# Optimization experiments

Hardware: AMD Instinct MI355X
Metric: run time of the kernel (lower is better)

Reference implementation:

```python
import jax, jax.numpy as jnp
import numpy as np

EMBED_DIM = 1024
NUM_HEADS = 16
HEAD_DIM = EMBED_DIM // NUM_HEADS  # 64
B, H_P, W_P = 4, 48, 48
N = H_P * W_P  # 2304


def setup_inputs() -> dict:
    key = jax.random.key(0)
    ks = jax.random.split(key, 12)
    s = 1.0 / np.sqrt(EMBED_DIM)
    inp = {
        "query": jax.random.normal(ks[0], (B, N, EMBED_DIM), jnp.float32),
        "key": jax.random.normal(ks[1], (B, N, EMBED_DIM), jnp.float32),
        "value": jax.random.normal(ks[2], (B, N, EMBED_DIM), jnp.float32),
        "Wq": jax.random.normal(ks[3], (EMBED_DIM, EMBED_DIM), jnp.float32) * s,
        "bq": jnp.zeros((EMBED_DIM,), jnp.float32),
        "Wk": jax.random.normal(ks[4], (EMBED_DIM, EMBED_DIM), jnp.float32) * s,
        "bk": jnp.zeros((EMBED_DIM,), jnp.float32),
        "Wv": jax.random.normal(ks[5], (EMBED_DIM, EMBED_DIM), jnp.float32) * s,
        "bv": jnp.zeros((EMBED_DIM,), jnp.float32),
        "Wo": jax.random.normal(ks[6], (EMBED_DIM, EMBED_DIM), jnp.float32) * s,
        "bo": jnp.zeros((EMBED_DIM,), jnp.float32),
        "H_patch": H_P,
        "W_patch": W_P,
    }
    return inp


def _rope_2d_cos_sin(h_idx, w_idx, head_dim):
    # 2D RoPE: first half of head_dim encodes the y axis, second half the x axis.
    half = head_dim // 2          # dims per spatial axis (32)
    inv_freq = 1.0 / (10000.0 ** (jnp.arange(0, half, 2, dtype=jnp.float32) / half))  # [half//2]
    fh = h_idx.astype(jnp.float32)[:, None] * inv_freq[None, :]  # [N, half//2]
    fw = w_idx.astype(jnp.float32)[:, None] * inv_freq[None, :]
    emb_h = jnp.concatenate([fh, fh], axis=-1)  # [N, half]
    emb_w = jnp.concatenate([fw, fw], axis=-1)
    emb = jnp.concatenate([emb_h, emb_w], axis=-1)  # [N, head_dim]
    return jnp.cos(emb), jnp.sin(emb)


def _rotate_half_seg(x):
    # rotate_half within a per-axis segment
    h = x.shape[-1] // 2
    return jnp.concatenate([-x[..., h:], x[..., :h]], axis=-1)


def _apply_rotary_2d(x, cos, sin):
    # x: [B, H, N, head_dim]; cos/sin: [N, head_dim]
    half = x.shape[-1] // 2
    c = cos[None, None]
    s = sin[None, None]
    xh, xw = x[..., :half], x[..., half:]
    ch, cw = c[..., :half], c[..., half:]
    sh, sw = s[..., :half], s[..., half:]
    yh = xh * ch + _rotate_half_seg(xh) * sh
    yw = xw * cw + _rotate_half_seg(xw) * sw
    return jnp.concatenate([yh, yw], axis=-1)


def reference(query, key, value, Wq, bq, Wk, bk, Wv, bv, Wo, bo, H_patch, W_patch):
    Bsz, Nn, D = query.shape
    hd = D // NUM_HEADS

    def split_heads(x):
        return x.reshape(Bsz, Nn, NUM_HEADS, hd).transpose(0, 2, 1, 3)  # [B,H,N,hd]

    q = split_heads(query @ Wq.T + bq)
    k = split_heads(key @ Wk.T + bk)
    v = split_heads(value @ Wv.T + bv)

    ys = jnp.arange(H_patch)
    xs = jnp.arange(W_patch)
    yy, xx = jnp.meshgrid(ys, xs, indexing="ij")
    cos, sin = _rope_2d_cos_sin(yy.reshape(-1), xx.reshape(-1), hd)

    q = _apply_rotary_2d(q, cos, sin)
    k = _apply_rotary_2d(k, cos, sin)

    scale = hd ** (-0.5)
    attn = jnp.einsum("bhnd,bhmd->bhnm", q, k) * scale
    attn = jax.nn.softmax(attn, axis=-1)
    out = jnp.einsum("bhnm,bhmd->bhnd", attn, v)
    out = out.transpose(0, 2, 1, 3).reshape(Bsz, Nn, D)
    return out @ Wo.T + bo
```

## Files before the change

### kernel.cpp

```cpp
#include <hip/hip_runtime.h>
#include <cstdint>
#include <cstddef>


typedef __bf16 bf16x8 __attribute__((ext_vector_type(8)));
typedef __bf16 bf16x4 __attribute__((ext_vector_type(4)));
typedef _Float16 f16x4 __attribute__((ext_vector_type(4)));
typedef float f32x4 __attribute__((ext_vector_type(4)));

constexpr int Bc = 4, Hc = 16, Nc = 2304, Ec = 1024, WPc = 48;
constexpr int BNc = Bc * Nc;

__device__ __forceinline__ f32x4 mfma16(bf16x8 a, bf16x8 b, f32x4 c) {
  return __builtin_amdgcn_mfma_f32_16x16x32_bf16(a, b, c, 0, 0, 0);
}
__device__ __forceinline__ f32x4 mfmah(f16x4 a, f16x4 b, f32x4 c) {
  return __builtin_amdgcn_mfma_f32_16x16x16f16(a, b, c, 0, 0, 0);
}

#define GPTR(p) ((const __attribute__((address_space(1))) void*)(p))
#define LPTR(p) ((__attribute__((address_space(3))) void*)(p))

__global__ __launch_bounds__(256) void cvt_bf16(const float* __restrict__ s,
                                                __bf16* __restrict__ d, int n) {
  int i = (blockIdx.x * 256 + threadIdx.x) * 8;
  if (i >= n) return;
  float4 f0 = *(const float4*)(s + i);
  float4 f1 = *(const float4*)(s + i + 4);
  bf16x8 v;
  v[0] = (__bf16)f0.x; v[1] = (__bf16)f0.y; v[2] = (__bf16)f0.z; v[3] = (__bf16)f0.w;
  v[4] = (__bf16)f1.x; v[5] = (__bf16)f1.y; v[6] = (__bf16)f1.z; v[7] = (__bf16)f1.w;
  *(bf16x8*)(d + i) = v;
}

#define GEMM_CORE(APTR, WPTR, KDIM)                                             \
  __shared__ __align__(16) __bf16 As[128 * 32];                                 \
  __shared__ __align__(16) __bf16 Bs[128 * 32];                                 \
  const int t = threadIdx.x;                                                    \
  const int lane = t & 63, wave = t >> 6;                                       \
  const int wm = wave & 1, wn = wave >> 1;                                      \
  const int quad = lane >> 4, l15 = lane & 15;                                  \
  const int rowInC = lane >> 2, colC = (lane & 3) * 8;                          \
  const __bf16* Ab = (APTR) + (size_t)(tm * 128) * (KDIM);                      \
  const __bf16* Wb = (WPTR) + (size_t)(tn * 128) * (KDIM);                      \
  f32x4 zero = {0.f, 0.f, 0.f, 0.f};                                            \
  f32x4 acc[4][4];                                                              \
  for (int i = 0; i < 4; ++i)                                                   \
    for (int j = 0; j < 4; ++j) acc[i][j] = zero;                               \
  for (int kk = 0; kk < (KDIM); kk += 32) {                                     \
    _Pragma("unroll") for (int tch = 0; tch < 2; ++tch) {                       \
      const int ch = wave * 2 + tch;                                            \
      const int row = ch * 16 + rowInC;                                         \
      __builtin_amdgcn_global_load_lds(GPTR(Ab + (size_t)row * (KDIM) + kk + colC), \
                                       LPTR(As + ch * 512), 16, 0, 0);          \
      __builtin_amdgcn_global_load_lds(GPTR(Wb + (size_t)row * (KDIM) + kk + colC), \
                                       LPTR(Bs + ch * 512), 16, 0, 0);          \
    }                                                                           \
    __syncthreads();                                                            \
    bf16x8 af[4], bfg[4];                                                       \
    _Pragma("unroll") for (int i = 0; i < 4; ++i)                               \
        af[i] = *(const bf16x8*)(As + (wm * 64 + i * 16 + l15) * 32 + quad * 8);\
    _Pragma("unroll") for (int j = 0; j < 4; ++j)                               \
        bfg[j] = *(const bf16x8*)(Bs + (wn * 64 + j * 16 + l15) * 32 + quad * 8);\
    _Pragma("unroll") for (int i = 0; i < 4; ++i)                               \
      _Pragma("unroll") for (int j = 0; j < 4; ++j)                             \
        acc[i][j] = mfma16(af[i], bfg[j], acc[i][j]);                           \
    __syncthreads();                                                            \
  }                                                                             \
  const int m0 = tm * 128 + wm * 64;                                            \
  const int nb0 = tn * 128 + wn * 64;

__global__ __launch_bounds__(256) void gemm_qk(const __bf16* __restrict__ qkb,
                                               const __bf16* __restrict__ Wqk,
                                               const float* __restrict__ bq,
                                               const float* __restrict__ bk,
                                               __bf16* __restrict__ Qhp,
                                               __bf16* __restrict__ Khp,
                                               float qscale) {
  const int tn = blockIdx.x & 15;
  const int tm = blockIdx.x >> 4;
  const int proj = tn >> 3;
  const __bf16* Asel = qkb + (size_t)proj * BNc * Ec;
  GEMM_CORE(Asel, Wqk, Ec)

  const int h = (nb0 >> 6) & 15;
  const float scale = proj ? 1.0f : qscale;
  __bf16* O = proj ? Khp : Qhp;
  const float* bb = proj ? bk : bq;
  float bj[4];
#pragma unroll
  for (int j = 0; j < 4; ++j) bj[j] = bb[(nb0 + j * 16 + l15) & 1023];
  const float f = exp2f(-(float)l15 * 0.8304820237218406f);
  const int lo3 = l15 & 7, hi8 = l15 >> 3;
#pragma unroll
  for (int i = 0; i < 4; ++i) {
#pragma unroll
    for (int r = 0; r < 4; ++r) {
      const int m = m0 + i * 16 + quad * 4 + r;
      const int b = m / Nc;
      const int ntok = m - b * Nc;
      const int ph = ntok / WPc, pw = ntok - (ntok / WPc) * WPc;
      float sh, ch, sw, cw;
      __sincosf((float)ph * f, &sh, &ch);
      __sincosf((float)pw * f, &sw, &cw);
      const float x0 = acc[i][0][r] + bj[0];
      const float x1 = acc[i][1][r] + bj[1];
      const float x2 = acc[i][2][r] + bj[2];
      const float x3 = acc[i][3][r] + bj[3];
      __bf16* Op = O + ((size_t)(b * Hc + h) * Nc + ntok) * 64;
      const int n7 = proj ? (ntok & 7) : 0;
      Op[(((0 + hi8) ^ n7) << 3) | lo3] = (__bf16)((x0 * ch - x1 * sh) * scale);
      Op[(((2 + hi8) ^ n7) << 3) | lo3] = (__bf16)((x1 * ch + x0 * sh) * scale);
      Op[(((4 + hi8) ^ n7) << 3) | lo3] = (__bf16)((x2 * cw - x3 * sw) * scale);
      Op[(((6 + hi8) ^ n7) << 3) | lo3] = (__bf16)((x3 * cw + x2 * sw) * scale);
    }
  }
}

__global__ __launch_bounds__(256) void gemm_v(const __bf16* __restrict__ A,
                                              const __bf16* __restrict__ Wv,
                                              const float* __restrict__ bv,
                                              _Float16* __restrict__ Vt) {
  const int tn = blockIdx.x & 7;
  const int tm = blockIdx.x >> 3;
  GEMM_CORE(A, Wv, Ec)

  const int h = nb0 >> 6;
#pragma unroll
  for (int i = 0; i < 4; ++i) {
    const int m = m0 + i * 16 + quad * 4;
    const int b = m / Nc;
    const int ntok = m - b * Nc;
    const int seg = ntok >> 6;
    const int cw = (ntok >> 2) & 15;
#pragma unroll
    for (int j = 0; j < 4; ++j) {
      const int d = j * 16 + l15;
      const float bi = bv[nb0 + j * 16 + l15];
      f16x4 v;
#pragma unroll
      for (int r = 0; r < 4; ++r) v[r] = (_Float16)(acc[i][j][r] + bi);
      const int off = seg * 64 + (((cw ^ l15) & 15) << 2);
      *(f16x4*)(Vt + ((size_t)(b * Hc + h) * 64 + d) * Nc + off) = v;
    }
  }
}

__global__ __launch_bounds__(256) void gemm_out(const __bf16* __restrict__ A,
                                                const __bf16* __restrict__ Wo,
                                                const float* __restrict__ bo,
                                                float* __restrict__ C) {
  const int tn = blockIdx.x & 7;
  const int tm = blockIdx.x >> 3;
  GEMM_CORE(A, Wo, Ec)

#pragma unroll
  for (int j = 0; j < 4; ++j) {
    const int n = nb0 + j * 16 + l15;
    const float bi = bo[n];
#pragma unroll
    for (int i = 0; i < 4; ++i) {
      const int m = m0 + i * 16 + quad * 4;
#pragma unroll
      for (int r = 0; r < 4; ++r) C[(size_t)(m + r) * Ec + n] = acc[i][j][r] + bi;
    }
  }
}

constexpr int TQ = 128, TK = 64, NT = Nc / TK;

__global__ __launch_bounds__(256) void attn(const __bf16* __restrict__ Qh,
                                            const __bf16* __restrict__ Kg,
                                            const _Float16* __restrict__ Vg,
                                            __bf16* __restrict__ Om) {
  const int bh = blockIdx.x;
  const int t = threadIdx.x, wave = t >> 6, lane = t & 63;
  const int quad = lane >> 4, l15 = lane & 15;

  __shared__ __align__(16) __bf16 Kls[2][TK * 64];
  __shared__ __align__(16) _Float16 Vls[2][TK * 64];

  const int qbase = blockIdx.y * TQ + wave * 32;
  bf16x8 bq[2][2];
#pragma unroll
  for (int s = 0; s < 2; ++s)
#pragma unroll
    for (int ks = 0; ks < 2; ++ks)
      bq[s][ks] = *(const bf16x8*)(Qh + ((size_t)bh * Nc + qbase + s * 16 + l15) * 64 +
                                   ks * 32 + quad * 8);

  const __bf16* Kbh = Kg + (size_t)bh * Nc * 64;
  const _Float16* Vbh = Vg + (size_t)bh * 64 * Nc;

  const f32x4 zero = {0.f, 0.f, 0.f, 0.f};
  f32x4 oacc[2][4] = {{zero, zero, zero, zero}, {zero, zero, zero, zero}};
  f32x4 osum[2] = {zero, zero};
  const f16x4 fones = {(_Float16)1.f, (_Float16)1.f, (_Float16)1.f, (_Float16)1.f};

  const int vrow = lane >> 3, vcol = (lane & 7) * 8;

#define STAGE(kt, buf)                                                          \
  {                                                                             \
    _Pragma("unroll") for (int i = 0; i < 2; ++i) {                             \
      const int ch = wave * 2 + i;                                              \
      __builtin_amdgcn_global_load_lds(                                         \
          GPTR(Kbh + (size_t)(kt) * TK * 64 + ch * 512 + lane * 8),             \
          LPTR(&Kls[buf][ch * 512]), 16, 0, 0);                                 \
    }                                                                           \
    _Pragma("unroll") for (int i = 0; i < 2; ++i) {                             \
      const int ch = wave * 2 + i;                                              \
      const int d = ch * 8 + vrow;                                              \
      __builtin_amdgcn_global_load_lds(                                         \
          GPTR(Vbh + (size_t)d * Nc + (kt) * 64 + vcol),                        \
          LPTR(&Vls[buf][ch * 512]), 16, 0, 0);                                 \
    }                                                                           \
  }

#define COMPUTE(BUF)                                                            \
  {                                                                             \
    f32x4 sacc[2][4] = {{zero, zero, zero, zero}, {zero, zero, zero, zero}};    \
    _Pragma("unroll") for (int ks = 0; ks < 2; ++ks) {                          \
      _Pragma("unroll") for (int ct = 0; ct < 4; ++ct) {                        \
        const bf16x8 ak = *(const bf16x8*)(&Kls[BUF][(ct * 16 + l15) * 64 +     \
            (((ks * 4 + quad) ^ (l15 & 7)) << 3)]);                             \
        sacc[0][ct] = mfma16(ak, bq[0][ks], sacc[0][ct]);                       \
        sacc[1][ct] = mfma16(ak, bq[1][ks], sacc[1][ct]);                       \
      }                                                                         \
    }                                                                           \
    f16x4 pf[2][4];                                                             \
    _Pragma("unroll") for (int s = 0; s < 2; ++s)                               \
      _Pragma("unroll") for (int ct = 0; ct < 4; ++ct)                          \
        _Pragma("unroll") for (int r = 0; r < 4; ++r)                           \
          pf[s][ct][r] = (_Float16)exp2f(sacc[s][ct][r]);                       \
    _Pragma("unroll") for (int ct = 0; ct < 4; ++ct) {                          \
      _Pragma("unroll") for (int dt = 0; dt < 4; ++dt) {                        \
        const f16x4 av = *(const f16x4*)(&Vls[BUF][(dt * 16 + l15) * 64 +       \
            (((ct * 4 + quad) ^ l15) << 2)]);                                   \
        oacc[0][dt] = mfmah(av, pf[0][ct], oacc[0][dt]);                        \
        oacc[1][dt] = mfmah(av, pf[1][ct], oacc[1][dt]);                        \
      }                                                                         \
      osum[0] = mfmah(fones, pf[0][ct], osum[0]);                               \
      osum[1] = mfmah(fones, pf[1][ct], osum[1]);                               \
    }                                                                           \
  }

  STAGE(0, 0);
  __syncthreads();

  for (int kt = 0; kt < NT; kt += 2) {
    STAGE(kt + 1, 1);
    COMPUTE(0)
    __syncthreads();
    if (kt + 2 < NT) STAGE(kt + 2, 0);
    COMPUTE(1)
    __syncthreads();
  }

  const int b = bh >> 4, h = bh & 15;
#pragma unroll
  for (int s = 0; s < 2; ++s) {
    const float rinv = 1.0f / osum[s][0];
    __bf16* Op = Om + ((size_t)b * Nc + qbase + s * 16 + l15) * Ec + h * 64 + quad * 4;
#pragma unroll
    for (int dt = 0; dt < 4; ++dt) {
      bf16x4 o;
#pragma unroll
      for (int r = 0; r < 4; ++r) o[r] = (__bf16)(oacc[s][dt][r] * rinv);
      *(bf16x4*)(Op + dt * 16) = o;
    }
  }
#undef STAGE
#undef COMPUTE
}

extern "C" void kernel_launch(void* const* d_in, const int* in_sizes, int n_in,
                              void* d_out, int out_size, void* d_ws, size_t ws_size,
                              hipStream_t stream) {
  const float* q  = (const float*)d_in[0];
  const float* k  = (const float*)d_in[1];
  const float* v  = (const float*)d_in[2];
  const float* Wq = (const float*)d_in[3];
  const float* bq = (const float*)d_in[4];
  const float* Wk = (const float*)d_in[5];
  const float* bk = (const float*)d_in[6];
  const float* Wv = (const float*)d_in[7];
  const float* bv = (const float*)d_in[8];
  const float* Wo = (const float*)d_in[9];
  const float* bo = (const float*)d_in[10];
  float* out = (float*)d_out;

  const size_t EE = (size_t)Ec * Ec;
  const size_t BNE = (size_t)BNc * Ec;

  char* w = (char*)d_ws;
  __bf16* Wqkb = (__bf16*)w; w += 2 * EE * 2;
  __bf16* Wvb  = (__bf16*)w; w += EE * 2;
  __bf16* Wob  = (__bf16*)w; w += EE * 2;
  __bf16* qb   = (__bf16*)w; w += BNE * 2;
  __bf16* kb   = (__bf16*)w; w += BNE * 2;
  __bf16* vb   = (__bf16*)w; w += BNE * 2;
  __bf16* Qhp  = (__bf16*)w; w += BNE * 2;
  __bf16* Khp  = (__bf16*)w; w += BNE * 2;
  _Float16* Vtp = (_Float16*)kb;
  __bf16* Omp = qb;

  const dim3 blk(256);
  const dim3 gCvtW(EE / 8 / 256);
  const dim3 gCvtA(BNE / 8 / 256);
  const dim3 gQK(16 * (BNc / 128));
  const dim3 gG(8 * (BNc / 128));
  const dim3 gAttn(Bc * Hc, Nc / TQ);

  cvt_bf16<<<gCvtW, blk, 0, stream>>>(Wq, Wqkb, (int)EE);
  cvt_bf16<<<gCvtW, blk, 0, stream>>>(Wk, Wqkb + EE, (int)EE);
  cvt_bf16<<<gCvtW, blk, 0, stream>>>(Wv, Wvb, (int)EE);
  cvt_bf16<<<gCvtW, blk, 0, stream>>>(Wo, Wob, (int)EE);
  cvt_bf16<<<gCvtA, blk, 0, stream>>>(q, qb, (int)BNE);
  cvt_bf16<<<gCvtA, blk, 0, stream>>>(k, kb, (int)BNE);
  cvt_bf16<<<gCvtA, blk, 0, stream>>>(v, vb, (int)BNE);

  const float qscale = 0.125f * 1.44269504088896340736f;

  gemm_qk<<<gQK, blk, 0, stream>>>(qb, Wqkb, bq, bk, Qhp, Khp, qscale);
  gemm_v<<<gG, blk, 0, stream>>>(vb, Wvb, bv, Vtp);
  attn<<<gAttn, blk, 0, stream>>>(Qhp, Khp, Vtp, Omp);
  gemm_out<<<gG, blk, 0, stream>>>(Omp, Wob, bo, out);
}
```

Before: 479.7 us.

## Triple-buffer GEMM and attention loops with one barrier per stage, use 32-wide f16 MFMA

The GEMM core and the attention loop move from double buffering with two __syncthreads per step to a three-stage LDS ring. Each phase waits with an explicit vmcnt, passes a single barrier, then prefetches two tiles ahead, and MFMA sections raise wave priority with setprio. The PV product switches from 16x16x16 f16 MFMA to 16x16x32, which needs 8-wide fragments, so the V-transpose store swizzle and the K token permutation are changed to match. This is meant to hide load latency and halve the instruction count for PV, at the cost of more LDS per block and fragile hand-counted waitcnt values.

```diff
diff --git a/kernel.cpp b/kernel.cpp
--- a/kernel.cpp
+++ b/kernel.cpp
@@ -6,6 +6,7 @@
 typedef __bf16 bf16x8 __attribute__((ext_vector_type(8)));
 typedef __bf16 bf16x4 __attribute__((ext_vector_type(4)));
 typedef _Float16 f16x4 __attribute__((ext_vector_type(4)));
+typedef _Float16 f16x8 __attribute__((ext_vector_type(8)));
 typedef float f32x4 __attribute__((ext_vector_type(4)));
 
 constexpr int Bc = 4, Hc = 16, Nc = 2304, Ec = 1024, WPc = 48;
@@ -14,8 +15,8 @@
 __device__ __forceinline__ f32x4 mfma16(bf16x8 a, bf16x8 b, f32x4 c) {
   return __builtin_amdgcn_mfma_f32_16x16x32_bf16(a, b, c, 0, 0, 0);
 }
-__device__ __forceinline__ f32x4 mfmah(f16x4 a, f16x4 b, f32x4 c) {
-  return __builtin_amdgcn_mfma_f32_16x16x16f16(a, b, c, 0, 0, 0);
+__device__ __forceinline__ f32x4 mfmah32(f16x8 a, f16x8 b, f32x4 c) {
+  return __builtin_amdgcn_mfma_f32_16x16x32_f16(a, b, c, 0, 0, 0);
 }
 
 #define GPTR(p) ((const __attribute__((address_space(1))) void*)(p))
@@ -33,40 +34,61 @@
   *(bf16x8*)(d + i) = v;
 }
 
+
+#define GSTAGE(KK, BUF)                                                         \
+  {                                                                             \
+    _Pragma("unroll") for (int tch = 0; tch < 2; ++tch) {                       \
+      const int ch = wave * 2 + tch;                                            \
+      const int row = ch * 16 + rowInC;                                         \
+      __builtin_amdgcn_global_load_lds(GPTR(Ab + (size_t)row * KD + (KK) + colC), \
+                                       LPTR(&As[BUF][ch * 512]), 16, 0, 0);     \
+      __builtin_amdgcn_global_load_lds(GPTR(Wb + (size_t)row * KD + (KK) + colC), \
+                                       LPTR(&Bs[BUF][ch * 512]), 16, 0, 0);     \
+    }                                                                           \
+  }
+
+#define GPHASE(KT, BUF, WN, DS)                                                 \
+  asm volatile("s_waitcnt vmcnt(" #WN ")" ::: "memory");                        \
+  __builtin_amdgcn_s_barrier();                                                 \
+  asm volatile("" ::: "memory");                                                \
+  if (DS) GSTAGE(((KT) + 2) * 32, ((BUF) + 2) % 3)                              \
+  {                                                                             \
+    bf16x8 af[4], bfg[4];                                                       \
+    _Pragma("unroll") for (int i = 0; i < 4; ++i)                               \
+        af[i] = *(const bf16x8*)(&As[BUF][(wm * 64 + i * 16 + l15) * 32 + quad * 8]); \
+    _Pragma("unroll") for (int j = 0; j < 4; ++j)                               \
+        bfg[j] = *(const bf16x8*)(&Bs[BUF][(wn * 64 + j * 16 + l15) * 32 + quad * 8]); \
+    __builtin_amdgcn_s_setprio(1);                                              \
+    _Pragma("unroll") for (int i = 0; i < 4; ++i)                               \
+      _Pragma("unroll") for (int j = 0; j < 4; ++j)                             \
+        acc[i][j] = mfma16(af[i], bfg[j], acc[i][j]);                           \
+    __builtin_amdgcn_s_setprio(0);                                              \
+  }
+
 #define GEMM_CORE(APTR, WPTR, KDIM)                                             \
-  __shared__ __align__(16) __bf16 As[128 * 32];                                 \
-  __shared__ __align__(16) __bf16 Bs[128 * 32];                                 \
+  __shared__ __align__(16) __bf16 As[3][128 * 32];                              \
+  __shared__ __align__(16) __bf16 Bs[3][128 * 32];                              \
   const int t = threadIdx.x;                                                    \
   const int lane = t & 63, wave = t >> 6;                                       \
   const int wm = wave & 1, wn = wave >> 1;                                      \
   const int quad = lane >> 4, l15 = lane & 15;                                  \
   const int rowInC = lane >> 2, colC = (lane & 3) * 8;                          \
-  const __bf16* Ab = (APTR) + (size_t)(tm * 128) * (KDIM);                      \
-  const __bf16* Wb = (WPTR) + (size_t)(tn * 128) * (KDIM);                      \
+  const int KD = (KDIM);                                                        \
+  const __bf16* Ab = (APTR) + (size_t)(tm * 128) * KD;                          \
+  const __bf16* Wb = (WPTR) + (size_t)(tn * 128) * KD;                          \
   f32x4 zero = {0.f, 0.f, 0.f, 0.f};                                            \
   f32x4 acc[4][4];                                                              \
   for (int i = 0; i < 4; ++i)                                                   \
     for (int j = 0; j < 4; ++j) acc[i][j] = zero;                               \
-  for (int kk = 0; kk < (KDIM); kk += 32) {                                     \
-    _Pragma("unroll") for (int tch = 0; tch < 2; ++tch) {                       \
-      const int ch = wave * 2 + tch;                                            \
-      const int row = ch * 16 + rowInC;                                         \
-      __builtin_amdgcn_global_load_lds(GPTR(Ab + (size_t)row * (KDIM) + kk + colC), \
-                                       LPTR(As + ch * 512), 16, 0, 0);          \
-      __builtin_amdgcn_global_load_lds(GPTR(Wb + (size_t)row * (KDIM) + kk + colC), \
-                                       LPTR(Bs + ch * 512), 16, 0, 0);          \
-    }                                                                           \
-    __syncthreads();                                                            \
-    bf16x8 af[4], bfg[4];                                                       \
-    _Pragma("unroll") for (int i = 0; i < 4; ++i)                               \
-        af[i] = *(const bf16x8*)(As + (wm * 64 + i * 16 + l15) * 32 + quad * 8);\
-    _Pragma("unroll") for (int j = 0; j < 4; ++j)                               \
-        bfg[j] = *(const bf16x8*)(Bs + (wn * 64 + j * 16 + l15) * 32 + quad * 8);\
-    _Pragma("unroll") for (int i = 0; i < 4; ++i)                               \
-      _Pragma("unroll") for (int j = 0; j < 4; ++j)                             \
-        acc[i][j] = mfma16(af[i], bfg[j], acc[i][j]);                           \
-    __syncthreads();                                                            \
+  GSTAGE(0, 0)                                                                  \
+  GSTAGE(32, 1)                                                                 \
+  _Pragma("unroll 1") for (int kt = 0; kt < KD / 32 - 2; kt += 3) {             \
+    GPHASE(kt, 0, 4, 1)                                                         \
+    GPHASE(kt + 1, 1, 4, 1)                                                     \
+    GPHASE(kt + 2, 2, 4, 1)                                                     \
   }                                                                             \
+  GPHASE(KD / 32 - 2, 0, 4, 0)                                                  \
+  GPHASE(KD / 32 - 1, 1, 0, 0)                                                  \
   const int m0 = tm * 128 + wm * 64;                                            \
   const int nb0 = tn * 128 + wn * 64;
 
@@ -107,8 +129,13 @@
       const float x1 = acc[i][1][r] + bj[1];
       const float x2 = acc[i][2][r] + bj[2];
       const float x3 = acc[i][3][r] + bj[3];
-      __bf16* Op = O + ((size_t)(b * Hc + h) * Nc + ntok) * 64;
-      const int n7 = proj ? (ntok & 7) : 0;
+      int wtok = ntok;
+      if (proj) {
+        const int t64 = ntok & 63;
+        wtok = (ntok & ~63) | (t64 & 35) | ((t64 & 4) << 2) | ((t64 & 24) >> 1);
+      }
+      __bf16* Op = O + ((size_t)(b * Hc + h) * Nc + wtok) * 64;
+      const int n7 = proj ? (wtok & 7) : 0;
       Op[(((0 + hi8) ^ n7) << 3) | lo3] = (__bf16)((x0 * ch - x1 * sh) * scale);
       Op[(((2 + hi8) ^ n7) << 3) | lo3] = (__bf16)((x1 * ch + x0 * sh) * scale);
       Op[(((4 + hi8) ^ n7) << 3) | lo3] = (__bf16)((x2 * cw - x3 * sw) * scale);
@@ -131,8 +158,8 @@
     const int m = m0 + i * 16 + quad * 4;
     const int b = m / Nc;
     const int ntok = m - b * Nc;
-    const int seg = ntok >> 6;
-    const int cw = (ntok >> 2) & 15;
+    const int base = (ntok >> 6) * 64 + (((ntok >> 2) & 1) << 2);
+    const int c8 = (ntok >> 3) & 7;
 #pragma unroll
     for (int j = 0; j < 4; ++j) {
       const int d = j * 16 + l15;
@@ -140,7 +167,7 @@
       f16x4 v;
 #pragma unroll
       for (int r = 0; r < 4; ++r) v[r] = (_Float16)(acc[i][j][r] + bi);
-      const int off = seg * 64 + (((cw ^ l15) & 15) << 2);
+      const int off = base + ((c8 ^ (l15 & 7)) << 3);
       *(f16x4*)(Vt + ((size_t)(b * Hc + h) * 64 + d) * Nc + off) = v;
     }
   }
@@ -177,8 +204,8 @@
   const int t = threadIdx.x, wave = t >> 6, lane = t & 63;
   const int quad = lane >> 4, l15 = lane & 15;
 
-  __shared__ __align__(16) __bf16 Kls[2][TK * 64];
-  __shared__ __align__(16) _Float16 Vls[2][TK * 64];
+  __shared__ __align__(16) __bf16 Kls[3][TK * 64];
+  __shared__ __align__(16) _Float16 Vls[3][TK * 64];
 
   const int qbase = blockIdx.y * TQ + wave * 32;
   bf16x8 bq[2][2];
@@ -188,6 +215,11 @@
     for (int ks = 0; ks < 2; ++ks)
       bq[s][ks] = *(const bf16x8*)(Qh + ((size_t)bh * Nc + qbase + s * 16 + l15) * 64 +
                                    ks * 32 + quad * 8);
+#pragma unroll
+  for (int s = 0; s < 2; ++s)
+#pragma unroll
+    for (int ks = 0; ks < 2; ++ks) asm volatile("" : "+v"(bq[s][ks]));
+  asm volatile("s_waitcnt vmcnt(0)" ::: "memory");
 
   const __bf16* Kbh = Kg + (size_t)bh * Nc * 64;
   const _Float16* Vbh = Vg + (size_t)bh * 64 * Nc;
@@ -195,30 +227,32 @@
   const f32x4 zero = {0.f, 0.f, 0.f, 0.f};
   f32x4 oacc[2][4] = {{zero, zero, zero, zero}, {zero, zero, zero, zero}};
   f32x4 osum[2] = {zero, zero};
-  const f16x4 fones = {(_Float16)1.f, (_Float16)1.f, (_Float16)1.f, (_Float16)1.f};
+  const f16x8 fones8 = {(_Float16)1.f, (_Float16)1.f, (_Float16)1.f, (_Float16)1.f,
+                        (_Float16)1.f, (_Float16)1.f, (_Float16)1.f, (_Float16)1.f};
 
   const int vrow = lane >> 3, vcol = (lane & 7) * 8;
 
-#define STAGE(kt, buf)                                                          \
+#define STAGE(KT2, BUF2)                                                        \
   {                                                                             \
     _Pragma("unroll") for (int i = 0; i < 2; ++i) {                             \
       const int ch = wave * 2 + i;                                              \
       __builtin_amdgcn_global_load_lds(                                         \
-          GPTR(Kbh + (size_t)(kt) * TK * 64 + ch * 512 + lane * 8),             \
-          LPTR(&Kls[buf][ch * 512]), 16, 0, 0);                                 \
+          GPTR(Kbh + (size_t)(KT2) * (TK * 64) + ch * 512 + lane * 8),          \
+          LPTR(&Kls[BUF2][ch * 512]), 16, 0, 0);                                \
     }                                                                           \
     _Pragma("unroll") for (int i = 0; i < 2; ++i) {                             \
       const int ch = wave * 2 + i;                                              \
       const int d = ch * 8 + vrow;                                              \
       __builtin_amdgcn_global_load_lds(                                         \
-          GPTR(Vbh + (size_t)d * Nc + (kt) * 64 + vcol),                        \
-          LPTR(&Vls[buf][ch * 512]), 16, 0, 0);                                 \
+          GPTR(Vbh + (size_t)d * Nc + (size_t)(KT2) * 64 + vcol),               \
+          LPTR(&Vls[BUF2][ch * 512]), 16, 0, 0);                                \
     }                                                                           \
   }
 
 #define COMPUTE(BUF)                                                            \
   {                                                                             \
     f32x4 sacc[2][4] = {{zero, zero, zero, zero}, {zero, zero, zero, zero}};    \
+    __builtin_amdgcn_s_setprio(1);                                              \
     _Pragma("unroll") for (int ks = 0; ks < 2; ++ks) {                          \
       _Pragma("unroll") for (int ct = 0; ct < 4; ++ct) {                        \
         const bf16x8 ak = *(const bf16x8*)(&Kls[BUF][(ct * 16 + l15) * 64 +     \
@@ -227,34 +261,48 @@
         sacc[1][ct] = mfma16(ak, bq[1][ks], sacc[1][ct]);                       \
       }                                                                         \
     }                                                                           \
-    f16x4 pf[2][4];                                                             \
+    __builtin_amdgcn_s_setprio(0);                                              \
+    f16x8 pf[2][2];                                                             \
     _Pragma("unroll") for (int s = 0; s < 2; ++s)                               \
-      _Pragma("unroll") for (int ct = 0; ct < 4; ++ct)                          \
-        _Pragma("unroll") for (int r = 0; r < 4; ++r)                           \
-          pf[s][ct][r] = (_Float16)exp2f(sacc[s][ct][r]);                       \
-    _Pragma("unroll") for (int ct = 0; ct < 4; ++ct) {                          \
+      _Pragma("unroll") for (int c2 = 0; c2 < 2; ++c2) {                        \
+        _Pragma("unroll") for (int r = 0; r < 4; ++r) {                         \
+          pf[s][c2][r]     = (_Float16)exp2f(sacc[s][2 * c2][r]);               \
+          pf[s][c2][4 + r] = (_Float16)exp2f(sacc[s][2 * c2 + 1][r]);           \
+        }                                                                       \
+      }                                                                         \
+    __builtin_amdgcn_s_setprio(1);                                              \
+    _Pragma("unroll") for (int c2 = 0; c2 < 2; ++c2) {                          \
       _Pragma("unroll") for (int dt = 0; dt < 4; ++dt) {                        \
-        const f16x4 av = *(const f16x4*)(&Vls[BUF][(dt * 16 + l15) * 64 +       \
-            (((ct * 4 + quad) ^ l15) << 2)]);                                   \
-        oacc[0][dt] = mfmah(av, pf[0][ct], oacc[0][dt]);                        \
-        oacc[1][dt] = mfmah(av, pf[1][ct], oacc[1][dt]);                        \
+        const f16x8 av = *(const f16x8*)(&Vls[BUF][(dt * 16 + l15) * 64 +       \
+            (((c2 * 4 + quad) ^ (l15 & 7)) << 3)]);                             \
+        oacc[0][dt] = mfmah32(av, pf[0][c2], oacc[0][dt]);                      \
+        oacc[1][dt] = mfmah32(av, pf[1][c2], oacc[1][dt]);                      \
       }                                                                         \
-      osum[0] = mfmah(fones, pf[0][ct], osum[0]);                               \
-      osum[1] = mfmah(fones, pf[1][ct], osum[1]);                               \
-    }                                                                           \
-  }
-
-  STAGE(0, 0);
-  __syncthreads();
-
-  for (int kt = 0; kt < NT; kt += 2) {
-    STAGE(kt + 1, 1);
-    COMPUTE(0)
-    __syncthreads();
-    if (kt + 2 < NT) STAGE(kt + 2, 0);
-    COMPUTE(1)
-    __syncthreads();
-  }
+      osum[0] = mfmah32(fones8, pf[0][c2], osum[0]);                            \
+      osum[1] = mfmah32(fones8, pf[1][c2], osum[1]);                            \
+    }                                                                           \
+    __builtin_amdgcn_s_setprio(0);                                              \
+  }
+
+#define PHASE(KT, BUF, WN, DS)                                                  \
+  asm volatile("s_waitcnt vmcnt(" #WN ")" ::: "memory");                        \
+  __builtin_amdgcn_s_barrier();                                                 \
+  asm volatile("" ::: "memory");                                                \
+  if (DS) STAGE((KT) + 2, ((BUF) + 2) % 3)                                      \
+  COMPUTE(BUF)
+
+  STAGE(0, 0)
+  STAGE(1, 1)
+
+#pragma unroll 1
+  for (int kt = 0; kt < NT - 3; kt += 3) {
+    PHASE(kt, 0, 4, 1)
+    PHASE(kt + 1, 1, 4, 1)
+    PHASE(kt + 2, 2, 4, 1)
+  }
+  PHASE(NT - 3, 0, 4, 1)
+  PHASE(NT - 2, 1, 4, 0)
+  PHASE(NT - 1, 2, 0, 0)
 
   const int b = bh >> 4, h = bh & 15;
 #pragma unroll
@@ -271,6 +319,7 @@
   }
 #undef STAGE
 #undef COMPUTE
+#undef PHASE
 }
 
 extern "C" void kernel_launch(void* const* d_in, const int* in_sizes, int n_in,
```

Measured after the change: 516.8 us. 7.7% more time.

## Pre-swizzle K/V into MFMA fragment layout and load directly to registers

Applied to the files above, without the earlier changes.

The QK and V projection epilogues now write K and V in a per-64-token tile layout that matches MFMA operand fragments, so the attention kernel loads them straight from global memory into registers with no LDS staging or __syncthreads. The PV product switches to the 16x16x32 f16 MFMA, and the MFMA blocks are wrapped in s_setprio hints. The seven conversion launches are also merged into one kernel that depends on the workspace buffers being contiguous. The aim is to cut LDS traffic, barriers and launch overhead, at the cost of losing K/V sharing across the four waves of a block, which raises global and L2 load traffic.

```diff
diff --git a/kernel.cpp b/kernel.cpp
--- a/kernel.cpp
+++ b/kernel.cpp
@@ -6,6 +6,7 @@
 typedef __bf16 bf16x8 __attribute__((ext_vector_type(8)));
 typedef __bf16 bf16x4 __attribute__((ext_vector_type(4)));
 typedef _Float16 f16x4 __attribute__((ext_vector_type(4)));
+typedef _Float16 f16x8 __attribute__((ext_vector_type(8)));
 typedef float f32x4 __attribute__((ext_vector_type(4)));
 
 constexpr int Bc = 4, Hc = 16, Nc = 2304, Ec = 1024, WPc = 48;
@@ -14,23 +15,38 @@
 __device__ __forceinline__ f32x4 mfma16(bf16x8 a, bf16x8 b, f32x4 c) {
   return __builtin_amdgcn_mfma_f32_16x16x32_bf16(a, b, c, 0, 0, 0);
 }
-__device__ __forceinline__ f32x4 mfmah(f16x4 a, f16x4 b, f32x4 c) {
-  return __builtin_amdgcn_mfma_f32_16x16x16f16(a, b, c, 0, 0, 0);
+__device__ __forceinline__ f32x4 mfmah32(f16x8 a, f16x8 b, f32x4 c) {
+  return __builtin_amdgcn_mfma_f32_16x16x32_f16(a, b, c, 0, 0, 0);
 }
 
 #define GPTR(p) ((const __attribute__((address_space(1))) void*)(p))
 #define LPTR(p) ((__attribute__((address_space(3))) void*)(p))
 
-__global__ __launch_bounds__(256) void cvt_bf16(const float* __restrict__ s,
-                                                __bf16* __restrict__ d, int n) {
-  int i = (blockIdx.x * 256 + threadIdx.x) * 8;
-  if (i >= n) return;
-  float4 f0 = *(const float4*)(s + i);
-  float4 f1 = *(const float4*)(s + i + 4);
+__global__ __launch_bounds__(256) void cvt_all(
+    const float* __restrict__ s0, const float* __restrict__ s1,
+    const float* __restrict__ s2, const float* __restrict__ s3,
+    const float* __restrict__ s4, const float* __restrict__ s5,
+    const float* __restrict__ s6, __bf16* __restrict__ d) {
+  const size_t EE = (size_t)Ec * Ec, BNE = (size_t)BNc * Ec;
+  const size_t g = ((size_t)blockIdx.x * 256 + threadIdx.x) * 8;
+  const float* s;
+  size_t off;
+  if (g < 4 * EE) {
+    const size_t a = g >> 20;
+    off = g & (EE - 1);
+    s = (a == 0) ? s0 : (a == 1) ? s1 : (a == 2) ? s2 : s3;
+  } else {
+    const size_t h = g - 4 * EE;
+    const size_t a = h / BNE;
+    off = h - a * BNE;
+    s = (a == 0) ? s4 : (a == 1) ? s5 : s6;
+  }
+  float4 f0 = *(const float4*)(s + off);
+  float4 f1 = *(const float4*)(s + off + 4);
   bf16x8 v;
   v[0] = (__bf16)f0.x; v[1] = (__bf16)f0.y; v[2] = (__bf16)f0.z; v[3] = (__bf16)f0.w;
   v[4] = (__bf16)f1.x; v[5] = (__bf16)f1.y; v[6] = (__bf16)f1.z; v[7] = (__bf16)f1.w;
-  *(bf16x8*)(d + i) = v;
+  *(bf16x8*)(d + g) = v;
 }
 
 #define GEMM_CORE(APTR, WPTR, KDIM)                                             \
@@ -84,8 +100,6 @@
   GEMM_CORE(Asel, Wqk, Ec)
 
   const int h = (nb0 >> 6) & 15;
-  const float scale = proj ? 1.0f : qscale;
-  __bf16* O = proj ? Khp : Qhp;
   const float* bb = proj ? bk : bq;
   float bj[4];
 #pragma unroll
@@ -107,12 +121,26 @@
       const float x1 = acc[i][1][r] + bj[1];
       const float x2 = acc[i][2][r] + bj[2];
       const float x3 = acc[i][3][r] + bj[3];
-      __bf16* Op = O + ((size_t)(b * Hc + h) * Nc + ntok) * 64;
-      const int n7 = proj ? (ntok & 7) : 0;
-      Op[(((0 + hi8) ^ n7) << 3) | lo3] = (__bf16)((x0 * ch - x1 * sh) * scale);
-      Op[(((2 + hi8) ^ n7) << 3) | lo3] = (__bf16)((x1 * ch + x0 * sh) * scale);
-      Op[(((4 + hi8) ^ n7) << 3) | lo3] = (__bf16)((x2 * cw - x3 * sw) * scale);
-      Op[(((6 + hi8) ^ n7) << 3) | lo3] = (__bf16)((x3 * cw + x2 * sw) * scale);
+      const float y0 = x0 * ch - x1 * sh;
+      const float y1 = x1 * ch + x0 * sh;
+      const float y2 = x2 * cw - x3 * sw;
+      const float y3 = x3 * cw + x2 * sw;
+      if (proj == 0) {
+        __bf16* Op = Qhp + ((size_t)(b * Hc + h) * Nc + ntok) * 64;
+        Op[l15]      = (__bf16)(y0 * qscale);
+        Op[l15 + 16] = (__bf16)(y1 * qscale);
+        Op[l15 + 32] = (__bf16)(y2 * qscale);
+        Op[l15 + 48] = (__bf16)(y3 * qscale);
+      } else {
+        const int t64 = ntok & 63;
+        const int p64 = (t64 & 35) | ((t64 & 4) << 2) | ((t64 & 24) >> 1);
+        __bf16* Kp = Khp + ((size_t)(b * Hc + h) * 36 + (ntok >> 6)) * 4096 +
+                     (size_t)((((p64 >> 4) * 2) * 64 + hi8 * 16 + (p64 & 15)) * 8 + lo3);
+        Kp[0]   = (__bf16)y0;
+        Kp[256] = (__bf16)y1;
+        Kp[512] = (__bf16)y2;
+        Kp[768] = (__bf16)y3;
+      }
     }
   }
 }
@@ -131,17 +159,17 @@
     const int m = m0 + i * 16 + quad * 4;
     const int b = m / Nc;
     const int ntok = m - b * Nc;
-    const int seg = ntok >> 6;
-    const int cw = (ntok >> 2) & 15;
+    const int t64 = ntok & 63;
+    const int c2 = t64 >> 5, qf = (t64 >> 3) & 3, jf0 = t64 & 7;
+    const size_t vbase = ((size_t)(b * Hc + h) * 36 + (ntok >> 6)) * 4096;
 #pragma unroll
     for (int j = 0; j < 4; ++j) {
-      const int d = j * 16 + l15;
       const float bi = bv[nb0 + j * 16 + l15];
       f16x4 v;
 #pragma unroll
       for (int r = 0; r < 4; ++r) v[r] = (_Float16)(acc[i][j][r] + bi);
-      const int off = seg * 64 + (((cw ^ l15) & 15) << 2);
-      *(f16x4*)(Vt + ((size_t)(b * Hc + h) * 64 + d) * Nc + off) = v;
+      *(f16x4*)(Vt + vbase +
+                (size_t)(((c2 * 4 + j) * 64 + qf * 16 + l15) * 8 + jf0)) = v;
     }
   }
 }
@@ -170,17 +198,14 @@
 constexpr int TQ = 128, TK = 64, NT = Nc / TK;
 
 __global__ __launch_bounds__(256) void attn(const __bf16* __restrict__ Qh,
-                                            const __bf16* __restrict__ Kg,
-                                            const _Float16* __restrict__ Vg,
+                                            const __bf16* __restrict__ Kf,
+                                            const _Float16* __restrict__ Vf,
                                             __bf16* __restrict__ Om) {
   const int bh = blockIdx.x;
   const int t = threadIdx.x, wave = t >> 6, lane = t & 63;
   const int quad = lane >> 4, l15 = lane & 15;
-
-  __shared__ __align__(16) __bf16 Kls[2][TK * 64];
-  __shared__ __align__(16) _Float16 Vls[2][TK * 64];
-
   const int qbase = blockIdx.y * TQ + wave * 32;
+
   bf16x8 bq[2][2];
 #pragma unroll
   for (int s = 0; s < 2; ++s)
@@ -189,71 +214,60 @@
       bq[s][ks] = *(const bf16x8*)(Qh + ((size_t)bh * Nc + qbase + s * 16 + l15) * 64 +
                                    ks * 32 + quad * 8);
 
-  const __bf16* Kbh = Kg + (size_t)bh * Nc * 64;
-  const _Float16* Vbh = Vg + (size_t)bh * 64 * Nc;
+  const __bf16* Kb = Kf + (size_t)bh * (NT * 4096) + (size_t)lane * 8;
+  const _Float16* Vb = Vf + (size_t)bh * (NT * 4096) + (size_t)lane * 8;
 
   const f32x4 zero = {0.f, 0.f, 0.f, 0.f};
   f32x4 oacc[2][4] = {{zero, zero, zero, zero}, {zero, zero, zero, zero}};
   f32x4 osum[2] = {zero, zero};
-  const f16x4 fones = {(_Float16)1.f, (_Float16)1.f, (_Float16)1.f, (_Float16)1.f};
-
-  const int vrow = lane >> 3, vcol = (lane & 7) * 8;
-
-#define STAGE(kt, buf)                                                          \
-  {                                                                             \
-    _Pragma("unroll") for (int i = 0; i < 2; ++i) {                             \
-      const int ch = wave * 2 + i;                                              \
-      __builtin_amdgcn_global_load_lds(                                         \
-          GPTR(Kbh + (size_t)(kt) * TK * 64 + ch * 512 + lane * 8),             \
-          LPTR(&Kls[buf][ch * 512]), 16, 0, 0);                                 \
-    }                                                                           \
-    _Pragma("unroll") for (int i = 0; i < 2; ++i) {                             \
-      const int ch = wave * 2 + i;                                              \
-      const int d = ch * 8 + vrow;                                              \
-      __builtin_amdgcn_global_load_lds(                                         \
-          GPTR(Vbh + (size_t)d * Nc + (kt) * 64 + vcol),                        \
-          LPTR(&Vls[buf][ch * 512]), 16, 0, 0);                                 \
-    }                                                                           \
-  }
-
-#define COMPUTE(BUF)                                                            \
-  {                                                                             \
-    f32x4 sacc[2][4] = {{zero, zero, zero, zero}, {zero, zero, zero, zero}};    \
-    _Pragma("unroll") for (int ks = 0; ks < 2; ++ks) {                          \
-      _Pragma("unroll") for (int ct = 0; ct < 4; ++ct) {                        \
-        const bf16x8 ak = *(const bf16x8*)(&Kls[BUF][(ct * 16 + l15) * 64 +     \
-            (((ks * 4 + quad) ^ (l15 & 7)) << 3)]);                             \
-        sacc[0][ct] = mfma16(ak, bq[0][ks], sacc[0][ct]);                       \
-        sacc[1][ct] = mfma16(ak, bq[1][ks], sacc[1][ct]);                       \
-      }                                                                         \
-    }                                                                           \
-    f16x4 pf[2][4];                                                             \
-    _Pragma("unroll") for (int s = 0; s < 2; ++s)                               \
-      _Pragma("unroll") for (int ct = 0; ct < 4; ++ct)                          \
-        _Pragma("unroll") for (int r = 0; r < 4; ++r)                           \
-          pf[s][ct][r] = (_Float16)exp2f(sacc[s][ct][r]);                       \
-    _Pragma("unroll") for (int ct = 0; ct < 4; ++ct) {                          \
-      _Pragma("unroll") for (int dt = 0; dt < 4; ++dt) {                        \
-        const f16x4 av = *(const f16x4*)(&Vls[BUF][(dt * 16 + l15) * 64 +       \
-            (((ct * 4 + quad) ^ l15) << 2)]);                                   \
-        oacc[0][dt] = mfmah(av, pf[0][ct], oacc[0][dt]);                        \
-        oacc[1][dt] = mfmah(av, pf[1][ct], oacc[1][dt]);                        \
-      }                                                                         \
-      osum[0] = mfmah(fones, pf[0][ct], osum[0]);                               \
-      osum[1] = mfmah(fones, pf[1][ct], osum[1]);                               \
-    }                                                                           \
-  }
-
-  STAGE(0, 0);
-  __syncthreads();
-
-  for (int kt = 0; kt < NT; kt += 2) {
-    STAGE(kt + 1, 1);
-    COMPUTE(0)
-    __syncthreads();
-    if (kt + 2 < NT) STAGE(kt + 2, 0);
-    COMPUTE(1)
-    __syncthreads();
+  const f16x8 fones8 = {(_Float16)1.f, (_Float16)1.f, (_Float16)1.f, (_Float16)1.f,
+                        (_Float16)1.f, (_Float16)1.f, (_Float16)1.f, (_Float16)1.f};
+
+  for (int kt = 0; kt < NT; ++kt) {
+    bf16x8 kf[8];
+#pragma unroll
+    for (int f = 0; f < 8; ++f)
+      kf[f] = *(const bf16x8*)(Kb + (size_t)kt * 4096 + f * 512);
+    f16x8 vfr[8];
+#pragma unroll
+    for (int f = 0; f < 8; ++f)
+      vfr[f] = *(const f16x8*)(Vb + (size_t)kt * 4096 + f * 512);
+
+    f32x4 sacc[2][4] = {{zero, zero, zero, zero}, {zero, zero, zero, zero}};
+    __builtin_amdgcn_s_setprio(1);
+#pragma unroll
+    for (int ks = 0; ks < 2; ++ks)
+#pragma unroll
+      for (int ct = 0; ct < 4; ++ct) {
+        sacc[0][ct] = mfma16(kf[ct * 2 + ks], bq[0][ks], sacc[0][ct]);
+        sacc[1][ct] = mfma16(kf[ct * 2 + ks], bq[1][ks], sacc[1][ct]);
+      }
+    __builtin_amdgcn_s_setprio(0);
+
+    f16x8 pf[2][2];
+#pragma unroll
+    for (int s = 0; s < 2; ++s)
+#pragma unroll
+      for (int c2 = 0; c2 < 2; ++c2) {
+#pragma unroll
+        for (int r = 0; r < 4; ++r) {
+          pf[s][c2][r]     = (_Float16)exp2f(sacc[s][2 * c2][r]);
+          pf[s][c2][4 + r] = (_Float16)exp2f(sacc[s][2 * c2 + 1][r]);
+        }
+      }
+
+    __builtin_amdgcn_s_setprio(1);
+#pragma unroll
+    for (int c2 = 0; c2 < 2; ++c2) {
+#pragma unroll
+      for (int dt = 0; dt < 4; ++dt) {
+        oacc[0][dt] = mfmah32(vfr[c2 * 4 + dt], pf[0][c2], oacc[0][dt]);
+        oacc[1][dt] = mfmah32(vfr[c2 * 4 + dt], pf[1][c2], oacc[1][dt]);
+      }
+      osum[0] = mfmah32(fones8, pf[0][c2], osum[0]);
+      osum[1] = mfmah32(fones8, pf[1][c2], osum[1]);
+    }
+    __builtin_amdgcn_s_setprio(0);
   }
 
   const int b = bh >> 4, h = bh & 15;
@@ -269,8 +283,6 @@
       *(bf16x4*)(Op + dt * 16) = o;
     }
   }
-#undef STAGE
-#undef COMPUTE
 }
 
 extern "C" void kernel_launch(void* const* d_in, const int* in_sizes, int n_in,
@@ -305,19 +317,12 @@
   __bf16* Omp = qb;
 
   const dim3 blk(256);
-  const dim3 gCvtW(EE / 8 / 256);
-  const dim3 gCvtA(BNE / 8 / 256);
+  const dim3 gCvt((4 * EE + 3 * BNE) / 8 / 256);
   const dim3 gQK(16 * (BNc / 128));
   const dim3 gG(8 * (BNc / 128));
   const dim3 gAttn(Bc * Hc, Nc / TQ);
 
-  cvt_bf16<<<gCvtW, blk, 0, stream>>>(Wq, Wqkb, (int)EE);
-  cvt_bf16<<<gCvtW, blk, 0, stream>>>(Wk, Wqkb + EE, (int)EE);
-  cvt_bf16<<<gCvtW, blk, 0, stream>>>(Wv, Wvb, (int)EE);
-  cvt_bf16<<<gCvtW, blk, 0, stream>>>(Wo, Wob, (int)EE);
-  cvt_bf16<<<gCvtA, blk, 0, stream>>>(q, qb, (int)BNE);
-  cvt_bf16<<<gCvtA, blk, 0, stream>>>(k, kb, (int)BNE);
-  cvt_bf16<<<gCvtA, blk, 0, stream>>>(v, vb, (int)BNE);
+  cvt_all<<<gCvt, blk, 0, stream>>>(Wq, Wk, Wv, Wo, q, k, v, Wqkb);
 
   const float qscale = 0.125f * 1.44269504088896340736f;
 
```

Measured after the change: 448.2 us. 1.07x faster.
